# Optimization experiments

Hardware: AMD Instinct MI355X
Metric: run time of the kernel (lower is better)

The kernel has to match this reference:

```python
import jax, jax.numpy as jnp
import numpy as np

B, H, W, C = 8, 512, 512, 32
BH = BW = 16
N_ACTIVE = 4096


def setup_inputs() -> dict:
    key = jax.random.key(0)
    k1, k2 = jax.random.split(key)
    x = jax.random.normal(k1, (N_ACTIVE, C, BH, BW), dtype=jnp.float32)
    y_base = jax.random.normal(k2, (B, H, W, C), dtype=jnp.float32)
    # unique block coordinates (n, yblk, xblk) so overwrite scatter is deterministic
    gh, gw = H // BH, W // BW  # 32, 32
    rng = np.random.default_rng(0)
    flat = rng.permutation(B * gh * gw)[:N_ACTIVE]
    n, yb, xb = np.unravel_index(flat, (B, gh, gw))
    indices = jnp.asarray(np.stack([n, yb, xb], axis=1), dtype=jnp.int32)
    return {
        "x": x, "y_base": y_base, "indices": indices,
        "bh": BH, "bw": BW, "sh": BH, "sw": BW, "oh": 0, "ow": 0,
    }


def reference(x, y_base, indices, bh, bw, sh, sw, oh, ow):
    # x: [N, C, bh, bw] -> NHWC blocks [N, bh, bw, C] (matches torch permute(0,2,3,1))
    xp = jnp.transpose(x, (0, 2, 3, 1))
    n = indices[:, 0]                                           # [N]
    r = indices[:, 1][:, None] * sh + oh + jnp.arange(bh)       # [N, bh]
    c = indices[:, 2][:, None] * sw + ow + jnp.arange(bw)       # [N, bw]
    # overwrite scatter (add=False): block values replace y_base at block locations
    y = y_base.at[n[:, None, None], r[:, :, None], c[:, None, :], :].set(xp)
    return y
```

## Files before the change

kernel.cpp:

```cpp
#include <hip/hip_runtime.h>

#define NBLK_TOTAL 8192
#define N_ACT      4096

__global__ __launch_bounds__(256) void build_map_kernel(const int* __restrict__ idx,
                                                        int* __restrict__ map) {
    int t = blockIdx.x * 256 + threadIdx.x;
    if (t < N_ACT) {
        int n  = idx[3 * t + 0];
        int yb = idx[3 * t + 1];
        int xb = idx[3 * t + 2];
        map[(n << 10) | (yb << 5) | xb] = t;
    }
}

__global__ __launch_bounds__(256) void scatter_kernel(const float* __restrict__ x,
                                                      const float* __restrict__ ybase,
                                                      const int* __restrict__ map,
                                                      float* __restrict__ out) {
    int b   = blockIdx.x;
    int src = map[b];
    int n   = b >> 10;
    int rem = b & 1023;
    int ybk = rem >> 5;
    int xbk = rem & 31;
    size_t base = (size_t)(n * 512 + ybk * 16) * 16384 + (size_t)(xbk * 16) * 32;
    int t = threadIdx.x;

    if (src < 0) {
        #pragma unroll
        for (int k = 0; k < 8; ++k) {
            int j = (k << 8) + t;
            int r = j >> 7;
            int p = j & 127;
            size_t off = base + (size_t)r * 16384 + (size_t)(p << 2);
            float4 v = *(const float4*)(ybase + off);
            *(float4*)(out + off) = v;
        }
    } else {
        __shared__ float lds[8192];
        const float4* xb4 = (const float4*)(x + (size_t)src * 8192);
        #pragma unroll
        for (int k = 0; k < 8; ++k) {
            int j  = (k << 8) + t;
            float4 v = xb4[j];
            int c  = j >> 6;
            int rc = (j & 63) << 2;
            int sw = (c >> 2) << 2;
            *(float4*)&lds[(c << 8) + (rc ^ sw)] = v;
        }
        __syncthreads();
        #pragma unroll
        for (int k = 0; k < 8; ++k) {
            int o4 = (k << 8) + t;
            int rc = o4 >> 3;
            int cq = (o4 & 7) << 2;
            float4 v;
            v.x = lds[((cq + 0) << 8) + (rc ^ cq)];
            v.y = lds[((cq + 1) << 8) + (rc ^ cq)];
            v.z = lds[((cq + 2) << 8) + (rc ^ cq)];
            v.w = lds[((cq + 3) << 8) + (rc ^ cq)];
            int r   = rc >> 4;
            int col = rc & 15;
            size_t off = base + (size_t)r * 16384 + (size_t)(col << 5) + cq;
            *(float4*)(out + off) = v;
        }
    }
}

extern "C" void kernel_launch(void* const* d_in, const int* in_sizes, int n_in,
                              void* d_out, int out_size, void* d_ws, size_t ws_size,
                              hipStream_t stream) {
    const float* x     = (const float*)d_in[0];
    const float* ybase = (const float*)d_in[1];
    const int*   idx   = (const int*)d_in[2];
    float* out = (float*)d_out;
    int*   map = (int*)d_ws;

    hipMemsetAsync(map, 0xFF, NBLK_TOTAL * sizeof(int), stream);
    build_map_kernel<<<N_ACT / 256, 256, 0, stream>>>(idx, map);
    scatter_kernel<<<NBLK_TOTAL, 256, 0, stream>>>(x, ybase, map, out);
}
```

Measured before the change: 505.4 us.

## Split scatter into active-block and inactive-copy kernels with nontemporal memory ops

Replaces the single per-output-block kernel with two kernels. One is launched per active input block, reads indices directly and does the LDS transpose. The other copies y_base only for blocks the map marks as inactive. This removes the divergent branch and the per-block map lookup from the active path, and lets the active scatter run without waiting for the map build. All global loads and stores now use nontemporal builtins to avoid cache pollution in this streaming workload. It adds an extra kernel launch and serializes two passes over the output.

```diff
diff --git a/kernel.cpp b/kernel.cpp
--- a/kernel.cpp
+++ b/kernel.cpp
@@ -2,6 +2,8 @@
 
 #define NBLK_TOTAL 8192
 #define N_ACT      4096
+
+typedef float f4 __attribute__((ext_vector_type(4)));
 
 __global__ __launch_bounds__(256) void build_map_kernel(const int* __restrict__ idx,
                                                         int* __restrict__ map) {
@@ -14,12 +16,52 @@
     }
 }
 
-__global__ __launch_bounds__(256) void scatter_kernel(const float* __restrict__ x,
-                                                      const float* __restrict__ ybase,
-                                                      const int* __restrict__ map,
-                                                      float* __restrict__ out) {
-    int b   = blockIdx.x;
-    int src = map[b];
+__global__ __launch_bounds__(256) void scatter_active_kernel(const float* __restrict__ x,
+                                                             const int* __restrict__ idx,
+                                                             float* __restrict__ out) {
+    int i   = blockIdx.x;
+    int n   = idx[3 * i + 0];
+    int ybk = idx[3 * i + 1];
+    int xbk = idx[3 * i + 2];
+    size_t base = (size_t)(n * 512 + ybk * 16) * 16384 + (size_t)(xbk * 16) * 32;
+    int t = threadIdx.x;
+
+    __shared__ float lds[8192];
+    const f4* xb4 = (const f4*)(x + (size_t)i * 8192);
+
+    #pragma unroll
+    for (int k = 0; k < 8; ++k) {
+        int j  = (k << 8) + t;
+        f4 v = __builtin_nontemporal_load(xb4 + j);
+        int c  = j >> 6;
+        int rc = (j & 63) << 2;
+        int sw = (c >> 2) << 2;
+        *(f4*)&lds[(c << 8) + (rc ^ sw)] = v;
+    }
+    __syncthreads();
+
+    #pragma unroll
+    for (int k = 0; k < 8; ++k) {
+        int o4 = (k << 8) + t;
+        int rc = o4 >> 3;
+        int cq = (o4 & 7) << 2;
+        f4 v;
+        v.x = lds[((cq + 0) << 8) + (rc ^ cq)];
+        v.y = lds[((cq + 1) << 8) + (rc ^ cq)];
+        v.z = lds[((cq + 2) << 8) + (rc ^ cq)];
+        v.w = lds[((cq + 3) << 8) + (rc ^ cq)];
+        int r   = rc >> 4;
+        int col = rc & 15;
+        size_t off = base + (size_t)r * 16384 + (size_t)(col << 5) + cq;
+        __builtin_nontemporal_store(v, (f4*)(out + off));
+    }
+}
+
+__global__ __launch_bounds__(256) void copy_inactive_kernel(const float* __restrict__ ybase,
+                                                            const int* __restrict__ map,
+                                                            float* __restrict__ out) {
+    int b = blockIdx.x;
+    if (map[b] >= 0) return;
     int n   = b >> 10;
     int rem = b & 1023;
     int ybk = rem >> 5;
@@ -27,44 +69,14 @@
     size_t base = (size_t)(n * 512 + ybk * 16) * 16384 + (size_t)(xbk * 16) * 32;
     int t = threadIdx.x;
 
-    if (src < 0) {
-        #pragma unroll
-        for (int k = 0; k < 8; ++k) {
-            int j = (k << 8) + t;
-            int r = j >> 7;
-            int p = j & 127;
-            size_t off = base + (size_t)r * 16384 + (size_t)(p << 2);
-            float4 v = *(const float4*)(ybase + off);
-            *(float4*)(out + off) = v;
-        }
-    } else {
-        __shared__ float lds[8192];
-        const float4* xb4 = (const float4*)(x + (size_t)src * 8192);
-        #pragma unroll
-        for (int k = 0; k < 8; ++k) {
-            int j  = (k << 8) + t;
-            float4 v = xb4[j];
-            int c  = j >> 6;
-            int rc = (j & 63) << 2;
-            int sw = (c >> 2) << 2;
-            *(float4*)&lds[(c << 8) + (rc ^ sw)] = v;
-        }
-        __syncthreads();
-        #pragma unroll
-        for (int k = 0; k < 8; ++k) {
-            int o4 = (k << 8) + t;
-            int rc = o4 >> 3;
-            int cq = (o4 & 7) << 2;
-            float4 v;
-            v.x = lds[((cq + 0) << 8) + (rc ^ cq)];
-            v.y = lds[((cq + 1) << 8) + (rc ^ cq)];
-            v.z = lds[((cq + 2) << 8) + (rc ^ cq)];
-            v.w = lds[((cq + 3) << 8) + (rc ^ cq)];
-            int r   = rc >> 4;
-            int col = rc & 15;
-            size_t off = base + (size_t)r * 16384 + (size_t)(col << 5) + cq;
-            *(float4*)(out + off) = v;
-        }
+    #pragma unroll
+    for (int k = 0; k < 8; ++k) {
+        int j = (k << 8) + t;
+        int r = j >> 7;
+        int p = j & 127;
+        size_t off = base + (size_t)r * 16384 + (size_t)(p << 2);
+        f4 v = __builtin_nontemporal_load((const f4*)(ybase + off));
+        __builtin_nontemporal_store(v, (f4*)(out + off));
     }
 }
 
@@ -77,7 +89,9 @@
     float* out = (float*)d_out;
     int*   map = (int*)d_ws;
 
-    hipMemsetAsync(map, 0xFF, NBLK_TOTAL * sizeof(int), stream);
+    scatter_active_kernel<<<N_ACT, 256, 0, stream>>>(x, idx, out);
+
+    (void)hipMemsetAsync(map, 0xFF, NBLK_TOTAL * sizeof(int), stream);
     build_map_kernel<<<N_ACT / 256, 256, 0, stream>>>(idx, map);
-    scatter_kernel<<<NBLK_TOTAL, 256, 0, stream>>>(x, ybase, map, out);
+    copy_inactive_kernel<<<NBLK_TOTAL, 256, 0, stream>>>(ybase, map, out);
 }
```

Result: faster. 491.5 us (-2.7%).
